# Performance work log

Measured on AMD Instinct MI355X. Metric: run time of the kernel, lower is better.

## Reference

```python
import jax, jax.numpy as jnp
import numpy as np

B, S, D_IN = 2, 2048, 1024
HIDDEN, H, HKV = 1024, 16, 4
R = H // HKV          # query heads per kv head
HD = HIDDEN // H      # head_dim = 64
D_OUT = 1024
SCALE = HD ** -0.5


def setup_inputs() -> dict:
    key = jax.random.key(0)
    ks = jax.random.split(key, 5)
    x = jax.random.normal(ks[0], (B, S, D_IN), dtype=jnp.float32)
    # store weights as (in, out); torch Linear computes x @ W.T with W (out,in)
    Wq = jax.random.normal(ks[1], (D_IN, HIDDEN), dtype=jnp.float32) * 0.02
    Wk = jax.random.normal(ks[2], (D_IN, HKV * HD), dtype=jnp.float32) * 0.02
    Wv = jax.random.normal(ks[3], (D_IN, HKV * HD), dtype=jnp.float32) * 0.02
    Wo = jax.random.normal(ks[4], (HIDDEN, D_OUT), dtype=jnp.float32) * 0.02
    return {"x": x, "Wq": Wq, "Wk": Wk, "Wv": Wv, "Wo": Wo}


def reference(x, Wq, Wk, Wv, Wo):
    # projections
    q = x @ Wq                                   # (B,S,H*HD)
    k = x @ Wk                                   # (B,S,HKV*HD)
    v = x @ Wv
    # repeat_interleave maps query head h -> kv head h // R,
    # so split query heads as (HKV, R) groups and broadcast KV.
    q = q.reshape(B, S, HKV, R, HD)
    k = k.reshape(B, S, HKV, HD)
    v = v.reshape(B, S, HKV, HD)
    attn = jnp.einsum('bskrd,btkd->bkrst', q, k) * SCALE   # (B,HKV,R,S,S)
    attn = jax.nn.softmax(attn, axis=-1)
    o = jnp.einsum('bkrst,btkd->bskrd', attn, v)           # (B,S,HKV,R,HD)
    o = o.reshape(B, S, HIDDEN)
    return o @ Wo                                          # (B,S,D_OUT)
```

## Files before the change

kernel.cpp:

```cpp
#include <hip/hip_runtime.h>

using u16 = unsigned short;
using u32 = unsigned int;
typedef __bf16 bf16x8 __attribute__((ext_vector_type(8)));
typedef u16 u16x8 __attribute__((ext_vector_type(8)));
typedef u32 u32x2 __attribute__((ext_vector_type(2)));
typedef u32 u32x4 __attribute__((ext_vector_type(4)));
typedef float f32x4 __attribute__((ext_vector_type(4)));
typedef float f32x16 __attribute__((ext_vector_type(16)));

#define B_   2
#define S_   2048
#define DIN  1024
#define HID  1024
#define NH   16
#define NKV  4
#define HD_  64
#define QKVW 1536
#define QSCL 0.1803368801111244f

__device__ __forceinline__ u16 f2b(float f) {
  u32 u = __builtin_bit_cast(u32, f);
  u32 r = (u + 0x7FFFu + ((u >> 16) & 1u)) >> 16;
  return (u16)r;
}

__device__ __forceinline__ void gl16(const void* g, void* l) {
  __builtin_amdgcn_global_load_lds(
      (const __attribute__((address_space(1))) void*)g,
      (__attribute__((address_space(3))) void*)l, 16, 0, 0);
}

__global__ void k_cvt(const float* __restrict__ in, u16* __restrict__ out, int n8) {
  int i = blockIdx.x * 256 + threadIdx.x;
  if (i >= n8) return;
  const float4* p = (const float4*)(in + (size_t)i * 8);
  float4 a = p[0], b = p[1];
  u16x8 o;
  o[0] = f2b(a.x); o[1] = f2b(a.y); o[2] = f2b(a.z); o[3] = f2b(a.w);
  o[4] = f2b(b.x); o[5] = f2b(b.y); o[6] = f2b(b.z); o[7] = f2b(b.w);
  *(u16x8*)(out + (size_t)i * 8) = o;
}

__global__ __launch_bounds__(256) void k_cvt_t(const float* __restrict__ W, u16* __restrict__ WT, int K, int N) {
  __shared__ float t[32][33];
  const int k0 = blockIdx.x * 32, n0 = blockIdx.y * 32;
  const int c = threadIdx.x & 31, r8 = threadIdx.x >> 5;
#pragma unroll
  for (int i = 0; i < 4; ++i)
    t[r8 + i * 8][c] = W[(size_t)(k0 + r8 + i * 8) * N + n0 + c];
  __syncthreads();
#pragma unroll
  for (int i = 0; i < 4; ++i)
    WT[(size_t)(n0 + r8 + i * 8) * K + k0 + c] = f2b(t[c][r8 + i * 8]);
}

__global__ __launch_bounds__(256) void k_vt(const u16* __restrict__ QKV, u16* __restrict__ Vt) {
  __shared__ u16 t[32][33];
  const int s0 = blockIdx.x * 32;
  const int d0 = blockIdx.y * 32;
  const int z  = blockIdx.z;
  const int b = z >> 2, kv = z & 3;
  const int c = threadIdx.x & 31, r8 = threadIdx.x >> 5;
#pragma unroll
  for (int i = 0; i < 4; ++i)
    t[r8 + i * 8][c] = QKV[(size_t)(b * S_ + s0 + r8 + i * 8) * QKVW + (HID + NKV * HD_) + kv * HD_ + d0 + c];
  __syncthreads();
#pragma unroll
  for (int i = 0; i < 4; ++i)
    Vt[(size_t)(z * HD_ + d0 + r8 + i * 8) * S_ + s0 + c] = t[c][r8 + i * 8];
}

template <typename OutT>
__global__ __launch_bounds__(256, 4) void k_gemm_bt(
    const u16* __restrict__ A, const u16* __restrict__ Bt,
    OutT* __restrict__ C, int M, int N, int K, int scaleCols, float scl)
{
  __shared__ u16 lA[2][128 * 32];
  __shared__ u16 lB[2][64 * 32];
  const int tid  = threadIdx.x;
  const int lane = tid & 63;
  const int wave = tid >> 6;
  const int wm = wave >> 1, wn = wave & 1;
  const int g = lane >> 4, li = lane & 15;
  const int bm = blockIdx.y * 128, bn = blockIdx.x * 64;
  const int arow = wave * 16 + (lane >> 2);
  const int acol = (lane & 3) * 8;

  f32x4 acc[4][2];
#pragma unroll
  for (int i = 0; i < 4; ++i)
#pragma unroll
    for (int j = 0; j < 2; ++j) acc[i][j] = f32x4{0.f, 0.f, 0.f, 0.f};

  const u16* Ab = A + (size_t)bm * K;
  const u16* Bb = Bt + (size_t)bn * K;

  auto stage = [&](int k0, int buf) {
#pragma unroll
    for (int h = 0; h < 2; ++h)
      gl16(&Ab[(size_t)(h * 64 + arow) * K + k0 + acol], (char*)lA[buf] + h * 4096 + wave * 1024);
    gl16(&Bb[(size_t)arow * K + k0 + acol], (char*)lB[buf] + wave * 1024);
  };

  stage(0, 0);
  __syncthreads();

  int cur = 0;
  for (int k0 = 0; k0 < K; k0 += 32) {
    if (k0 + 32 < K) stage(k0 + 32, cur ^ 1);
    bf16x8 af[4], bfr[2];
#pragma unroll
    for (int mt = 0; mt < 4; ++mt)
      af[mt] = *(const bf16x8*)&lA[cur][(wm * 64 + mt * 16 + li) * 32 + g * 8];
#pragma unroll
    for (int nt = 0; nt < 2; ++nt)
      bfr[nt] = *(const bf16x8*)&lB[cur][(wn * 32 + nt * 16 + li) * 32 + g * 8];
    __builtin_amdgcn_s_setprio(1);
#pragma unroll
    for (int mt = 0; mt < 4; ++mt)
#pragma unroll
      for (int nt = 0; nt < 2; ++nt)
        acc[mt][nt] = __builtin_amdgcn_mfma_f32_16x16x32_bf16(af[mt], bfr[nt], acc[mt][nt], 0, 0, 0);
    __builtin_amdgcn_s_setprio(0);
    __syncthreads();
    cur ^= 1;
  }

#pragma unroll
  for (int mt = 0; mt < 4; ++mt)
#pragma unroll
    for (int nt = 0; nt < 2; ++nt)
#pragma unroll
      for (int r = 0; r < 4; ++r) {
        int row = bm + wm * 64 + mt * 16 + g * 4 + r;
        int col = bn + wn * 32 + nt * 16 + li;
        float v = acc[mt][nt][r];
        if (col < scaleCols) v *= scl;
        if constexpr (sizeof(OutT) == 4) C[(size_t)row * N + col] = v;
        else                             C[(size_t)row * N + col] = f2b(v);
      }
}

__global__ __launch_bounds__(256, 2) void k_attn(
    const u16* __restrict__ QKV, const u16* __restrict__ Vt_g, u16* __restrict__ O)
{
  __shared__ u16 K_lds[2][64 * 64];
  __shared__ u16 Vt_lds[2][64 * 64];
  const int tid  = threadIdx.x;
  const int lane = tid & 63;
  const int w    = tid >> 6;
  const int lq = lane & 31;
  const int hi = lane >> 5;
  const int swl = (lq & 7) << 3;
  const int hx = (hi * 8) ^ (swl & 8);
  const int s0 = blockIdx.x * 32;
  const int kv = blockIdx.y;
  const int b  = blockIdx.z;
  const int hq = kv * 4 + w;

  int dcol[4];
#pragma unroll
  for (int d0 = 0; d0 < 4; ++d0) dcol[d0] = (d0 * 16) ^ (swl & 48);

  bf16x8 qf[4];
  {
    const u16* qb = QKV + (size_t)(b * S_ + s0 + lq) * QKVW + hq * HD_ + hi * 8;
#pragma unroll
    for (int d0 = 0; d0 < 4; ++d0) qf[d0] = *(const bf16x8*)(qb + d0 * 16);
  }

  float l = 0.f;
  f32x16 oacc0 = {}, oacc1 = {};

  const int sr8 = lane >> 3;
  const int scol = ((lane & 7) ^ sr8) * 8;
  const int srow = w * 16;
  const u16* kge = QKV + (size_t)(b * S_) * QKVW + HID + kv * HD_;
  const u16* vge = Vt_g + (size_t)((b * NKV + kv) * HD_) * S_;

  auto stage = [&](int t, int buf) {
#pragma unroll
    for (int h = 0; h < 2; ++h) {
      gl16(kge + (size_t)(t * 64 + srow + h * 8 + sr8) * QKVW + scol,
           (char*)K_lds[buf] + srow * 128 + h * 1024);
      gl16(vge + (size_t)(srow + h * 8 + sr8) * S_ + t * 64 + scol,
           (char*)Vt_lds[buf] + srow * 128 + h * 1024);
    }
  };

  stage(0, 0);
  __syncthreads();

  constexpr int NT = S_ / 64;
  for (int t = 0; t < NT; ++t) {
    const int cur = t & 1;
    if (t + 1 < NT) stage(t + 1, cur ^ 1);

    f32x16 st0 = {}, st1 = {};
    __builtin_amdgcn_s_setprio(1);
#pragma unroll
    for (int d0 = 0; d0 < 4; ++d0) {
      bf16x8 kf0 = *(const bf16x8*)&K_lds[cur][lq * 64 + dcol[d0] + hx];
      bf16x8 kf1 = *(const bf16x8*)&K_lds[cur][(32 + lq) * 64 + dcol[d0] + hx];
      st0 = __builtin_amdgcn_mfma_f32_32x32x16_bf16(kf0, qf[d0], st0, 0, 0, 0);
      st1 = __builtin_amdgcn_mfma_f32_32x32x16_bf16(kf1, qf[d0], st1, 0, 0, 0);
    }
    __builtin_amdgcn_s_setprio(0);

#pragma unroll
    for (int i = 0; i < 16; ++i) st0[i] = __builtin_amdgcn_exp2f(st0[i]);
#pragma unroll
    for (int i = 0; i < 16; ++i) st1[i] = __builtin_amdgcn_exp2f(st1[i]);
    float s8[8];
#pragma unroll
    for (int i = 0; i < 8; ++i)
      s8[i] = (st0[i] + st0[i + 8]) + (st1[i] + st1[i + 8]);
    s8[0] += s8[4]; s8[1] += s8[5]; s8[2] += s8[6]; s8[3] += s8[7];
    l += (s8[0] + s8[1]) + (s8[2] + s8[3]);

    bf16x8 pa[4];
#define PK(dst, x, y) asm("v_cvt_pk_bf16_f32 %0, %1, %2" : "=v"(dst) : "v"(x), "v"(y))
#pragma unroll
    for (int kb2 = 0; kb2 < 2; ++kb2) {
      const f32x16& ev = kb2 ? st1 : st0;
      u32 a0, a1, b0, b1;
      u32x2 r0, r1;
      u32x4 wv;
      PK(a0, ev[0], ev[1]);  PK(a1, ev[2], ev[3]);
      PK(b0, ev[4], ev[5]);  PK(b1, ev[6], ev[7]);
      r0 = __builtin_amdgcn_permlane32_swap(a0, b0, false, false);
      r1 = __builtin_amdgcn_permlane32_swap(a1, b1, false, false);
      wv[0] = r0[0]; wv[1] = r1[0]; wv[2] = r0[1]; wv[3] = r1[1];
      pa[kb2 * 2] = __builtin_bit_cast(bf16x8, wv);
      PK(a0, ev[8],  ev[9]);  PK(a1, ev[10], ev[11]);
      PK(b0, ev[12], ev[13]); PK(b1, ev[14], ev[15]);
      r0 = __builtin_amdgcn_permlane32_swap(a0, b0, false, false);
      r1 = __builtin_amdgcn_permlane32_swap(a1, b1, false, false);
      wv[0] = r0[0]; wv[1] = r1[0]; wv[2] = r0[1]; wv[3] = r1[1];
      pa[kb2 * 2 + 1] = __builtin_bit_cast(bf16x8, wv);
    }
#undef PK

    __builtin_amdgcn_s_setprio(1);
#pragma unroll
    for (int ks = 0; ks < 4; ++ks) {
      bf16x8 vf0 = *(const bf16x8*)&Vt_lds[cur][lq * 64 + dcol[ks] + hx];
      bf16x8 vf1 = *(const bf16x8*)&Vt_lds[cur][(32 + lq) * 64 + dcol[ks] + hx];
      oacc0 = __builtin_amdgcn_mfma_f32_32x32x16_bf16(pa[ks], vf0, oacc0, 0, 0, 0);
      oacc1 = __builtin_amdgcn_mfma_f32_32x32x16_bf16(pa[ks], vf1, oacc1, 0, 0, 0);
    }
    __builtin_amdgcn_s_setprio(0);

    __syncthreads();
  }

  l += __shfl_xor(l, 32);
  const size_t obase = (size_t)(b * S_ + s0) * HID + hq * HD_ + lq;
#pragma unroll
  for (int r = 0; r < 16; ++r) {
    const int qrow = (r & 3) + 8 * (r >> 2) + 4 * hi;
    float lr = __shfl(l, qrow);
    float inv = __builtin_amdgcn_rcpf(lr);
    O[obase + (size_t)qrow * HID]      = f2b(oacc0[r] * inv);
    O[obase + (size_t)qrow * HID + 32] = f2b(oacc1[r] * inv);
  }
}

extern "C" void kernel_launch(void* const* d_in, const int* in_sizes, int n_in,
                              void* d_out, int out_size, void* d_ws, size_t ws_size,
                              hipStream_t stream) {
  (void)in_sizes; (void)n_in; (void)out_size; (void)ws_size;
  const float* x  = (const float*)d_in[0];
  const float* Wq = (const float*)d_in[1];
  const float* Wk = (const float*)d_in[2];
  const float* Wv = (const float*)d_in[3];
  const float* Wo = (const float*)d_in[4];
  float* out = (float*)d_out;

  const size_t M = (size_t)B_ * S_;
  u16* xb    = (u16*)d_ws;
  u16* WqkvT = xb    + M * DIN;
  u16* WoT   = WqkvT + (size_t)QKVW * DIN;
  u16* QKV   = WoT   + (size_t)HID * HID;
  u16* Ob    = QKV   + M * QKVW;
  u16* Vt    = Ob    + M * HID;

  k_cvt<<<dim3((int)(M * DIN / 8 / 256)), 256, 0, stream>>>(x, xb, (int)(M * DIN / 8));
  k_cvt_t<<<dim3(DIN / 32, HID / 32),       256, 0, stream>>>(Wq, WqkvT,                      DIN, HID);
  k_cvt_t<<<dim3(DIN / 32, (NKV*HD_) / 32), 256, 0, stream>>>(Wk, WqkvT + (size_t)HID * DIN,  DIN, NKV * HD_);
  k_cvt_t<<<dim3(DIN / 32, (NKV*HD_) / 32), 256, 0, stream>>>(Wv, WqkvT + (size_t)(HID + NKV*HD_) * DIN, DIN, NKV * HD_);
  k_cvt_t<<<dim3(HID / 32, HID / 32),       256, 0, stream>>>(Wo, WoT, HID, HID);

  k_gemm_bt<u16><<<dim3(QKVW / 64, (int)(M / 128)), 256, 0, stream>>>(
      xb, WqkvT, QKV, (int)M, QKVW, DIN, HID, QSCL);

  k_vt<<<dim3(S_ / 32, HD_ / 32, B_ * NKV), 256, 0, stream>>>(QKV, Vt);

  k_attn<<<dim3(S_ / 32, NKV, B_), 256, 0, stream>>>(QKV, Vt, Ob);

  k_gemm_bt<float><<<dim3(HID / 64, (int)(M / 128)), 256, 0, stream>>>(
      Ob, WoT, out, (int)M, HID, HID, 0, 1.0f);
}
```

Baseline: 110.7 us.

## Software-pipeline PV MFMA one tile behind QK and merge QKV weight conversions

The attention loop now issues the P·V MFMAs for the previous tile right after the QK^T MFMAs of the current tile, so matrix work overlaps the exp/pack phase. This needs a triple-buffered K/V LDS ring and a drain step after the loop. The three Wq/Wk/Wv transpose-convert launches are also fused into one kernel to cut launch overhead. LDS use grows from 32 KB to 48 KB per block, which may reduce occupancy relative to the 2-blocks-per-CU launch bound, and the pa fragments now stay live across iterations, raising register pressure.

New measurement: 107.4 us. -3.0%, faster.

```diff
diff --git a/kernel.cpp b/kernel.cpp
--- a/kernel.cpp
+++ b/kernel.cpp
@@ -40,6 +40,26 @@
   o[0] = f2b(a.x); o[1] = f2b(a.y); o[2] = f2b(a.z); o[3] = f2b(a.w);
   o[4] = f2b(b.x); o[5] = f2b(b.y); o[6] = f2b(b.z); o[7] = f2b(b.w);
   *(u16x8*)(out + (size_t)i * 8) = o;
+}
+
+__global__ __launch_bounds__(256) void k_cvt_t3(
+    const float* __restrict__ Wq, const float* __restrict__ Wk,
+    const float* __restrict__ Wv, u16* __restrict__ WT)
+{
+  __shared__ float t[32][33];
+  const int k0 = blockIdx.x * 32, n0 = blockIdx.y * 32;
+  const float* W; int N, nb;
+  if (n0 < HID)             { W = Wq; N = HID; nb = n0; }
+  else if (n0 < HID + 256)  { W = Wk; N = 256; nb = n0 - HID; }
+  else                      { W = Wv; N = 256; nb = n0 - HID - 256; }
+  const int c = threadIdx.x & 31, r8 = threadIdx.x >> 5;
+#pragma unroll
+  for (int i = 0; i < 4; ++i)
+    t[r8 + i * 8][c] = W[(size_t)(k0 + r8 + i * 8) * N + nb + c];
+  __syncthreads();
+#pragma unroll
+  for (int i = 0; i < 4; ++i)
+    WT[(size_t)(n0 + r8 + i * 8) * DIN + k0 + c] = f2b(t[c][r8 + i * 8]);
 }
 
 __global__ __launch_bounds__(256) void k_cvt_t(const float* __restrict__ W, u16* __restrict__ WT, int K, int N) {
@@ -145,8 +165,8 @@
 __global__ __launch_bounds__(256, 2) void k_attn(
     const u16* __restrict__ QKV, const u16* __restrict__ Vt_g, u16* __restrict__ O)
 {
-  __shared__ u16 K_lds[2][64 * 64];
-  __shared__ u16 Vt_lds[2][64 * 64];
+  __shared__ u16 K_lds[3][64 * 64];
+  __shared__ u16 Vt_lds[3][64 * 64];
   const int tid  = threadIdx.x;
   const int lane = tid & 63;
   const int w    = tid >> 6;
@@ -172,6 +192,7 @@
 
   float l = 0.f;
   f32x16 oacc0 = {}, oacc1 = {};
+  bf16x8 pa[4];
 
   const int sr8 = lane >> 3;
   const int scol = ((lane & 7) ^ sr8) * 8;
@@ -192,21 +213,24 @@
   stage(0, 0);
   __syncthreads();
 
+#define PK(dst, x, y) asm("v_cvt_pk_bf16_f32 %0, %1, %2" : "=v"(dst) : "v"(x), "v"(y))
   constexpr int NT = S_ / 64;
+  int cb = 0;
   for (int t = 0; t < NT; ++t) {
-    const int cur = t & 1;
-    if (t + 1 < NT) stage(t + 1, cur ^ 1);
+    int nb = cb + 1; if (nb == 3) nb = 0;
+    int pb = cb - 1; if (pb < 0) pb = 2;
+    if (t + 1 < NT) stage(t + 1, nb);
 
     f32x16 st0 = {}, st1 = {};
+    const u16* Kc = K_lds[cb];
     __builtin_amdgcn_s_setprio(1);
 #pragma unroll
     for (int d0 = 0; d0 < 4; ++d0) {
-      bf16x8 kf0 = *(const bf16x8*)&K_lds[cur][lq * 64 + dcol[d0] + hx];
-      bf16x8 kf1 = *(const bf16x8*)&K_lds[cur][(32 + lq) * 64 + dcol[d0] + hx];
+      bf16x8 kf0 = *(const bf16x8*)&Kc[lq * 64 + dcol[d0] + hx];
+      bf16x8 kf1 = *(const bf16x8*)&Kc[(32 + lq) * 64 + dcol[d0] + hx];
       st0 = __builtin_amdgcn_mfma_f32_32x32x16_bf16(kf0, qf[d0], st0, 0, 0, 0);
       st1 = __builtin_amdgcn_mfma_f32_32x32x16_bf16(kf1, qf[d0], st1, 0, 0, 0);
     }
-    __builtin_amdgcn_s_setprio(0);
 
 #pragma unroll
     for (int i = 0; i < 16; ++i) st0[i] = __builtin_amdgcn_exp2f(st0[i]);
@@ -219,8 +243,18 @@
     s8[0] += s8[4]; s8[1] += s8[5]; s8[2] += s8[6]; s8[3] += s8[7];
     l += (s8[0] + s8[1]) + (s8[2] + s8[3]);
 
-    bf16x8 pa[4];
-#define PK(dst, x, y) asm("v_cvt_pk_bf16_f32 %0, %1, %2" : "=v"(dst) : "v"(x), "v"(y))
+    if (t > 0) {
+      const u16* Vc = Vt_lds[pb];
+#pragma unroll
+      for (int ks = 0; ks < 4; ++ks) {
+        bf16x8 vf0 = *(const bf16x8*)&Vc[lq * 64 + dcol[ks] + hx];
+        bf16x8 vf1 = *(const bf16x8*)&Vc[(32 + lq) * 64 + dcol[ks] + hx];
+        oacc0 = __builtin_amdgcn_mfma_f32_32x32x16_bf16(pa[ks], vf0, oacc0, 0, 0, 0);
+        oacc1 = __builtin_amdgcn_mfma_f32_32x32x16_bf16(pa[ks], vf1, oacc1, 0, 0, 0);
+      }
+    }
+    __builtin_amdgcn_s_setprio(0);
+
 #pragma unroll
     for (int kb2 = 0; kb2 < 2; ++kb2) {
       const f32x16& ev = kb2 ? st1 : st0;
@@ -240,19 +274,24 @@
       wv[0] = r0[0]; wv[1] = r1[0]; wv[2] = r0[1]; wv[3] = r1[1];
       pa[kb2 * 2 + 1] = __builtin_bit_cast(bf16x8, wv);
     }
+
+    __syncthreads();
+    cb = nb;
+  }
 #undef PK
 
+  {
+    int pb = cb - 1; if (pb < 0) pb = 2;
+    const u16* Vc = Vt_lds[pb];
     __builtin_amdgcn_s_setprio(1);
 #pragma unroll
     for (int ks = 0; ks < 4; ++ks) {
-      bf16x8 vf0 = *(const bf16x8*)&Vt_lds[cur][lq * 64 + dcol[ks] + hx];
-      bf16x8 vf1 = *(const bf16x8*)&Vt_lds[cur][(32 + lq) * 64 + dcol[ks] + hx];
+      bf16x8 vf0 = *(const bf16x8*)&Vc[lq * 64 + dcol[ks] + hx];
+      bf16x8 vf1 = *(const bf16x8*)&Vc[(32 + lq) * 64 + dcol[ks] + hx];
       oacc0 = __builtin_amdgcn_mfma_f32_32x32x16_bf16(pa[ks], vf0, oacc0, 0, 0, 0);
       oacc1 = __builtin_amdgcn_mfma_f32_32x32x16_bf16(pa[ks], vf1, oacc1, 0, 0, 0);
     }
     __builtin_amdgcn_s_setprio(0);
-
-    __syncthreads();
   }
 
   l += __shfl_xor(l, 32);
@@ -287,10 +326,8 @@
   u16* Vt    = Ob    + M * HID;
 
   k_cvt<<<dim3((int)(M * DIN / 8 / 256)), 256, 0, stream>>>(x, xb, (int)(M * DIN / 8));
-  k_cvt_t<<<dim3(DIN / 32, HID / 32),       256, 0, stream>>>(Wq, WqkvT,                      DIN, HID);
-  k_cvt_t<<<dim3(DIN / 32, (NKV*HD_) / 32), 256, 0, stream>>>(Wk, WqkvT + (size_t)HID * DIN,  DIN, NKV * HD_);
-  k_cvt_t<<<dim3(DIN / 32, (NKV*HD_) / 32), 256, 0, stream>>>(Wv, WqkvT + (size_t)(HID + NKV*HD_) * DIN, DIN, NKV * HD_);
-  k_cvt_t<<<dim3(HID / 32, HID / 32),       256, 0, stream>>>(Wo, WoT, HID, HID);
+  k_cvt_t3<<<dim3(DIN / 32, QKVW / 32), 256, 0, stream>>>(Wq, Wk, Wv, WqkvT);
+  k_cvt_t<<<dim3(HID / 32, HID / 32),   256, 0, stream>>>(Wo, WoT, HID, HID);
 
   k_gemm_bt<u16><<<dim3(QKVW / 64, (int)(M / 128)), 256, 0, stream>>>(
       xb, WqkvT, QKV, (int)M, QKVW, DIN, HID, QSCL);
```

## Enlarge attention tiles to 64 queries x 128 keys with 8 waves; fuse QKV weight transposes

Applied to the files above, without the earlier changes.

The attention kernel now uses 512-thread blocks covering 64 query rows (two groups of 4 heads), and each iteration stages 128 keys instead of 64. Every K/V tile loaded into LDS is therefore shared by twice as many waves, and the number of barriers and loop iterations is halved. The LDS swizzle for V is reworked to fit the wider tile. Separately, the three Wq/Wk/Wv transpose-convert launches are merged into one kernel to cut launch overhead. In exchange the attention grid has half as many blocks (256), and each block uses more LDS and registers, which may lower occupancy.

Result: faster. 107.6 us (-2.8%).

```diff
diff --git a/kernel.cpp b/kernel.cpp
--- a/kernel.cpp
+++ b/kernel.cpp
@@ -40,6 +40,26 @@
   o[0] = f2b(a.x); o[1] = f2b(a.y); o[2] = f2b(a.z); o[3] = f2b(a.w);
   o[4] = f2b(b.x); o[5] = f2b(b.y); o[6] = f2b(b.z); o[7] = f2b(b.w);
   *(u16x8*)(out + (size_t)i * 8) = o;
+}
+
+__global__ __launch_bounds__(256) void k_cvt_t3(
+    const float* __restrict__ Wq, const float* __restrict__ Wk,
+    const float* __restrict__ Wv, u16* __restrict__ WT)
+{
+  __shared__ float t[32][33];
+  const int k0 = blockIdx.x * 32, n0 = blockIdx.y * 32;
+  const float* W; int N, nb;
+  if (n0 < HID)             { W = Wq; N = HID; nb = n0; }
+  else if (n0 < HID + 256)  { W = Wk; N = 256; nb = n0 - HID; }
+  else                      { W = Wv; N = 256; nb = n0 - HID - 256; }
+  const int c = threadIdx.x & 31, r8 = threadIdx.x >> 5;
+#pragma unroll
+  for (int i = 0; i < 4; ++i)
+    t[r8 + i * 8][c] = W[(size_t)(k0 + r8 + i * 8) * N + nb + c];
+  __syncthreads();
+#pragma unroll
+  for (int i = 0; i < 4; ++i)
+    WT[(size_t)(n0 + r8 + i * 8) * DIN + k0 + c] = f2b(t[c][r8 + i * 8]);
 }
 
 __global__ __launch_bounds__(256) void k_cvt_t(const float* __restrict__ W, u16* __restrict__ WT, int K, int N) {
@@ -142,30 +162,26 @@
       }
 }
 
-__global__ __launch_bounds__(256, 2) void k_attn(
+__global__ __launch_bounds__(512, 2) void k_attn(
     const u16* __restrict__ QKV, const u16* __restrict__ Vt_g, u16* __restrict__ O)
 {
-  __shared__ u16 K_lds[2][64 * 64];
-  __shared__ u16 Vt_lds[2][64 * 64];
+  __shared__ u16 K_lds[2][128 * 64];
+  __shared__ u16 Vt_lds[2][64 * 128];
   const int tid  = threadIdx.x;
   const int lane = tid & 63;
   const int w    = tid >> 6;
   const int lq = lane & 31;
   const int hi = lane >> 5;
   const int swl = (lq & 7) << 3;
-  const int hx = (hi * 8) ^ (swl & 8);
-  const int s0 = blockIdx.x * 32;
+  const int s0 = blockIdx.x * 64;
   const int kv = blockIdx.y;
   const int b  = blockIdx.z;
-  const int hq = kv * 4 + w;
-
-  int dcol[4];
-#pragma unroll
-  for (int d0 = 0; d0 < 4; ++d0) dcol[d0] = (d0 * 16) ^ (swl & 48);
+  const int hq = kv * 4 + (w & 3);
+  const int wq = w >> 2;
 
   bf16x8 qf[4];
   {
-    const u16* qb = QKV + (size_t)(b * S_ + s0 + lq) * QKVW + hq * HD_ + hi * 8;
+    const u16* qb = QKV + (size_t)(b * S_ + s0 + wq * 32 + lq) * QKVW + hq * HD_ + hi * 8;
 #pragma unroll
     for (int d0 = 0; d0 < 4; ++d0) qf[d0] = *(const bf16x8*)(qb + d0 * 16);
   }
@@ -173,57 +189,65 @@
   float l = 0.f;
   f32x16 oacc0 = {}, oacc1 = {};
 
-  const int sr8 = lane >> 3;
-  const int scol = ((lane & 7) ^ sr8) * 8;
-  const int srow = w * 16;
   const u16* kge = QKV + (size_t)(b * S_) * QKVW + HID + kv * HD_;
   const u16* vge = Vt_g + (size_t)((b * NKV + kv) * HD_) * S_;
+  const int krow_l = (lane >> 3);
+  const int ksrc_c = ((lane & 7) ^ (lane >> 3)) * 8;
+  const int vrow_l = (lane >> 4);
+  const int vsw    = ((w * 4 + (lane >> 4)) & 7);
+  const int vsrc_c = ((lane & 15) ^ vsw) * 8;
 
   auto stage = [&](int t, int buf) {
 #pragma unroll
     for (int h = 0; h < 2; ++h) {
-      gl16(kge + (size_t)(t * 64 + srow + h * 8 + sr8) * QKVW + scol,
-           (char*)K_lds[buf] + srow * 128 + h * 1024);
-      gl16(vge + (size_t)(srow + h * 8 + sr8) * S_ + t * 64 + scol,
-           (char*)Vt_lds[buf] + srow * 128 + h * 1024);
+      gl16(kge + (size_t)(t * 128 + h * 64 + w * 8 + krow_l) * QKVW + ksrc_c,
+           (char*)K_lds[buf] + (h * 512 + w * 64) * 16);
+      gl16(vge + (size_t)(h * 32 + w * 4 + vrow_l) * S_ + t * 128 + vsrc_c,
+           (char*)Vt_lds[buf] + (h * 512 + w * 64) * 16);
     }
   };
 
   stage(0, 0);
   __syncthreads();
 
-  constexpr int NT = S_ / 64;
+#define PK(dst, x, y) asm("v_cvt_pk_bf16_f32 %0, %1, %2" : "=v"(dst) : "v"(x), "v"(y))
+  constexpr int NT = S_ / 128;
   for (int t = 0; t < NT; ++t) {
     const int cur = t & 1;
     if (t + 1 < NT) stage(t + 1, cur ^ 1);
 
-    f32x16 st0 = {}, st1 = {};
+    f32x16 st0 = {}, st1 = {}, st2 = {}, st3 = {};
+    const u16* Kc = K_lds[cur];
     __builtin_amdgcn_s_setprio(1);
 #pragma unroll
     for (int d0 = 0; d0 < 4; ++d0) {
-      bf16x8 kf0 = *(const bf16x8*)&K_lds[cur][lq * 64 + dcol[d0] + hx];
-      bf16x8 kf1 = *(const bf16x8*)&K_lds[cur][(32 + lq) * 64 + dcol[d0] + hx];
+      const int dc = (d0 * 16 + hi * 8) ^ swl;
+      bf16x8 kf0 = *(const bf16x8*)&Kc[(lq)       * 64 + dc];
+      bf16x8 kf1 = *(const bf16x8*)&Kc[(32 + lq)  * 64 + dc];
+      bf16x8 kf2 = *(const bf16x8*)&Kc[(64 + lq)  * 64 + dc];
+      bf16x8 kf3 = *(const bf16x8*)&Kc[(96 + lq)  * 64 + dc];
       st0 = __builtin_amdgcn_mfma_f32_32x32x16_bf16(kf0, qf[d0], st0, 0, 0, 0);
       st1 = __builtin_amdgcn_mfma_f32_32x32x16_bf16(kf1, qf[d0], st1, 0, 0, 0);
+      st2 = __builtin_amdgcn_mfma_f32_32x32x16_bf16(kf2, qf[d0], st2, 0, 0, 0);
+      st3 = __builtin_amdgcn_mfma_f32_32x32x16_bf16(kf3, qf[d0], st3, 0, 0, 0);
     }
     __builtin_amdgcn_s_setprio(0);
 
-#pragma unroll
-    for (int i = 0; i < 16; ++i) st0[i] = __builtin_amdgcn_exp2f(st0[i]);
-#pragma unroll
-    for (int i = 0; i < 16; ++i) st1[i] = __builtin_amdgcn_exp2f(st1[i]);
-    float s8[8];
-#pragma unroll
-    for (int i = 0; i < 8; ++i)
-      s8[i] = (st0[i] + st0[i + 8]) + (st1[i] + st1[i + 8]);
-    s8[0] += s8[4]; s8[1] += s8[5]; s8[2] += s8[6]; s8[3] += s8[7];
-    l += (s8[0] + s8[1]) + (s8[2] + s8[3]);
-
-    bf16x8 pa[4];
-#define PK(dst, x, y) asm("v_cvt_pk_bf16_f32 %0, %1, %2" : "=v"(dst) : "v"(x), "v"(y))
-#pragma unroll
-    for (int kb2 = 0; kb2 < 2; ++kb2) {
-      const f32x16& ev = kb2 ? st1 : st0;
+    auto expsum = [&](f32x16& s) {
+#pragma unroll
+      for (int i = 0; i < 16; ++i) s[i] = __builtin_amdgcn_exp2f(s[i]);
+      float a = 0.f, c = 0.f;
+#pragma unroll
+      for (int i = 0; i < 8; ++i) { a += s[i]; c += s[i + 8]; }
+      return a + c;
+    };
+    l += expsum(st0) + expsum(st1);
+    l += expsum(st2) + expsum(st3);
+
+    bf16x8 pa[8];
+#pragma unroll
+    for (int kb = 0; kb < 4; ++kb) {
+      const f32x16& ev = (kb == 0) ? st0 : (kb == 1) ? st1 : (kb == 2) ? st2 : st3;
       u32 a0, a1, b0, b1;
       u32x2 r0, r1;
       u32x4 wv;
@@ -232,21 +256,22 @@
       r0 = __builtin_amdgcn_permlane32_swap(a0, b0, false, false);
       r1 = __builtin_amdgcn_permlane32_swap(a1, b1, false, false);
       wv[0] = r0[0]; wv[1] = r1[0]; wv[2] = r0[1]; wv[3] = r1[1];
-      pa[kb2 * 2] = __builtin_bit_cast(bf16x8, wv);
+      pa[kb * 2] = __builtin_bit_cast(bf16x8, wv);
       PK(a0, ev[8],  ev[9]);  PK(a1, ev[10], ev[11]);
       PK(b0, ev[12], ev[13]); PK(b1, ev[14], ev[15]);
       r0 = __builtin_amdgcn_permlane32_swap(a0, b0, false, false);
       r1 = __builtin_amdgcn_permlane32_swap(a1, b1, false, false);
       wv[0] = r0[0]; wv[1] = r1[0]; wv[2] = r0[1]; wv[3] = r1[1];
-      pa[kb2 * 2 + 1] = __builtin_bit_cast(bf16x8, wv);
+      pa[kb * 2 + 1] = __builtin_bit_cast(bf16x8, wv);
     }
-#undef PK
-
+
+    const u16* Vc = Vt_lds[cur];
     __builtin_amdgcn_s_setprio(1);
 #pragma unroll
-    for (int ks = 0; ks < 4; ++ks) {
-      bf16x8 vf0 = *(const bf16x8*)&Vt_lds[cur][lq * 64 + dcol[ks] + hx];
-      bf16x8 vf1 = *(const bf16x8*)&Vt_lds[cur][(32 + lq) * 64 + dcol[ks] + hx];
+    for (int ks = 0; ks < 8; ++ks) {
+      const int vc = (ks * 16 + hi * 8) ^ swl;
+      bf16x8 vf0 = *(const bf16x8*)&Vc[(lq)      * 128 + vc];
+      bf16x8 vf1 = *(const bf16x8*)&Vc[(32 + lq) * 128 + vc];
       oacc0 = __builtin_amdgcn_mfma_f32_32x32x16_bf16(pa[ks], vf0, oacc0, 0, 0, 0);
       oacc1 = __builtin_amdgcn_mfma_f32_32x32x16_bf16(pa[ks], vf1, oacc1, 0, 0, 0);
     }
@@ -254,9 +279,10 @@
 
     __syncthreads();
   }
+#undef PK
 
   l += __shfl_xor(l, 32);
-  const size_t obase = (size_t)(b * S_ + s0) * HID + hq * HD_ + lq;
+  const size_t obase = (size_t)(b * S_ + s0 + wq * 32) * HID + hq * HD_ + lq;
 #pragma unroll
   for (int r = 0; r < 16; ++r) {
     const int qrow = (r & 3) + 8 * (r >> 2) + 4 * hi;
@@ -287,17 +313,15 @@
   u16* Vt    = Ob    + M * HID;
 
   k_cvt<<<dim3((int)(M * DIN / 8 / 256)), 256, 0, stream>>>(x, xb, (int)(M * DIN / 8));
-  k_cvt_t<<<dim3(DIN / 32, HID / 32),       256, 0, stream>>>(Wq, WqkvT,                      DIN, HID);
-  k_cvt_t<<<dim3(DIN / 32, (NKV*HD_) / 32), 256, 0, stream>>>(Wk, WqkvT + (size_t)HID * DIN,  DIN, NKV * HD_);
-  k_cvt_t<<<dim3(DIN / 32, (NKV*HD_) / 32), 256, 0, stream>>>(Wv, WqkvT + (size_t)(HID + NKV*HD_) * DIN, DIN, NKV * HD_);
-  k_cvt_t<<<dim3(HID / 32, HID / 32),       256, 0, stream>>>(Wo, WoT, HID, HID);
+  k_cvt_t3<<<dim3(DIN / 32, QKVW / 32), 256, 0, stream>>>(Wq, Wk, Wv, WqkvT);
+  k_cvt_t<<<dim3(HID / 32, HID / 32),   256, 0, stream>>>(Wo, WoT, HID, HID);
 
   k_gemm_bt<u16><<<dim3(QKVW / 64, (int)(M / 128)), 256, 0, stream>>>(
       xb, WqkvT, QKV, (int)M, QKVW, DIN, HID, QSCL);
 
   k_vt<<<dim3(S_ / 32, HD_ / 32, B_ * NKV), 256, 0, stream>>>(QKV, Vt);
 
-  k_attn<<<dim3(S_ / 32, NKV, B_), 256, 0, stream>>>(QKV, Vt, Ob);
+  k_attn<<<dim3(S_ / 64, NKV, B_), 512, 0, stream>>>(QKV, Vt, Ob);
 
   k_gemm_bt<float><<<dim3(HID / 64, (int)(M / 128)), 256, 0, stream>>>(
       Ob, WoT, out, (int)M, HID, HID, 0, 1.0f);
```
